# Kernel optimization log

Measured on AMD Instinct MI355X. Metric: run time of the kernel, lower is better.

The kernel has to match this reference:

```python
import jax, jax.numpy as jnp
import numpy as np

# ---- constants hard-coded in the torch module ----
NEG_EPS = 1e-30          # eps used in log clamps
TAU = 0.35               # near-field temperature (getattr default)
K0 = 128                 # near-field band width
C_EMBD, N_HEADS, RANK = 768, 12, 32
B, T = 1, 2048


def _lin(k, fin, fout):
    lim = 1.0 / np.sqrt(fin)
    return jax.random.uniform(k, (fin, fout), jnp.float32, -lim, lim)


def _bias(k, fin, fout):
    lim = 1.0 / np.sqrt(fin)
    return jax.random.uniform(k, (fout,), jnp.float32, -lim, lim)


def setup_inputs() -> dict:
    key = jax.random.key(0)
    ks = jax.random.split(key, 24)
    C, H, R = C_EMBD, N_HEADS, RANK
    return {
        "x": jax.random.normal(ks[0], (B, T, C), jnp.float32),
        "Wq_w": _lin(ks[1], C, C), "Wq_b": _bias(ks[2], C, C),
        "Wk_w": _lin(ks[3], C, C), "Wk_b": _bias(ks[4], C, C),
        "Wv_w": _lin(ks[5], C, C), "Wv_b": _bias(ks[6], C, C),
        "Wo_w": _lin(ks[7], C, C), "Wo_b": _bias(ks[8], C, C),
        "Pq_w": _lin(ks[9], C, R),
        "Pk_w": _lin(ks[10], C, R),
        "Pv_w": _lin(ks[11], C, R),
        "up_w": _lin(ks[12], R, C),
        "gate_u": jax.random.normal(ks[13], (H, C // H), jnp.float32),
        "gate_b": jnp.zeros((H,), jnp.float32),
        "Wz_w": _lin(ks[14], 4 * C, C), "Wz_b": _bias(ks[15], 4 * C, C),
    }


def reference(x, Wq_w, Wq_b, Wk_w, Wk_b, Wv_w, Wv_b, Wo_w, Wo_b,
              Pq_w, Pk_w, Pv_w, up_w, gate_u, gate_b, Wz_w, Wz_b):
    Bx, Tx, C = x.shape
    H = gate_u.shape[0]
    D = C // H
    R = Pq_w.shape[1]
    k0 = min(K0, Tx - 1)
    kernel = k0 + 1
    b_scalar = -np.log(max(Tx, 1)).astype(np.float32) if hasattr(np.log(1.0), 'astype') else -np.log(max(Tx, 1))
    b_scalar = jnp.float32(-np.log(max(Tx, 1)))

    # 0) projections + heads
    Q = x @ Wq_w + Wq_b
    K = x @ Wk_w + Wk_b
    V = x @ Wv_w + Wv_b
    heads = lambda z: z.reshape(Bx, Tx, H, D).transpose(0, 2, 1, 3)  # (B,H,T,D)
    Qh, Kh, Vh = heads(Q), heads(K), heads(V)

    idx = jnp.arange(Tx)
    causal = idx[None, :] <= idx[:, None]                  # (T,T)
    band = causal & ((idx[:, None] - idx[None, :]) <= k0)  # banded causal

    # 1) low-rank EA + sigmoid + LASER seed
    Qr, Kr, Vr = Q @ Pq_w, K @ Pk_w, V @ Pv_w              # (B,T,R)
    S = (Qr @ Kr.transpose(0, 2, 1)) * (1.0 / np.sqrt(R))  # (B,T,T)
    # masked logits were -1e9 -> sigmoid == 0 exactly in fp32
    A_seed = jnp.where(causal[None], jax.nn.sigmoid(S * S + b_scalar), 0.0)
    # running causal max over keys, per feature (== amax of causally masked keys)
    m_seed = jax.lax.cummax(Vr, axis=1)                    # (B,T,R)
    Yr = jnp.einsum('bij,bjr->bir', A_seed, jnp.exp(Vr)) * jnp.exp(-m_seed)
    H0 = (jnp.log(jnp.maximum(Yr, NEG_EPS)) + m_seed) @ up_w  # (B,T,C)

    # 2a) near-field banded causal attention (cos^2 / tau, sigmoid, LASER)
    l2n = lambda z: z / jnp.maximum(jnp.linalg.norm(z, axis=-1, keepdims=True), 1e-12)
    cos = jnp.einsum('bhid,bhjd->bhij', l2n(Qh), l2n(Kh))  # (B,H,T,T)
    A_near = jnp.where(band[None, None], jax.nn.sigmoid(cos * cos / TAU + b_scalar), 0.0)
    # sliding-window (width kernel, past-only) max of V per feature
    m_near = jax.lax.reduce_window(
        Vh, -jnp.inf, jax.lax.max,
        window_dimensions=(1, 1, kernel, 1), window_strides=(1, 1, 1, 1),
        padding=[(0, 0), (0, 0), (kernel - 1, 0), (0, 0)])   # (B,H,T,D)
    V_exp = jnp.exp(Vh - m_near)
    Y_near = jnp.einsum('bhij,bhjd->bhid', A_near, V_exp)
    H_near = jnp.log(jnp.maximum(Y_near, NEG_EPS)) + m_near

    # 2b) far-field hierarchical levels: source truncates mid-loop; the
    # accumulator H_far_total_h is initialized to zeros -> contributes zero.
    Ht_h = H_near                                          # (B,H,T,D)

    # 3) head-wise sigmoid gating
    g = jax.nn.sigmoid(jnp.einsum('bhtd,hd->bht', Ht_h, gate_u) + gate_b[None, :, None])
    Ht_h = Ht_h * g[..., None]
    Htilde = Ht_h.transpose(0, 2, 1, 3).reshape(Bx, Tx, C)

    # 4) GRU blend (Wz consumes 4*C features)
    z = jax.nn.sigmoid(jnp.concatenate([x, H0, Htilde, H0 * Htilde], axis=-1) @ Wz_w + Wz_b)
    H_out = (1.0 - z) * H0 + z * Htilde
    return H_out @ Wo_w + Wo_b
```

## Files before the change

### kernel.cpp

```cpp
#include <hip/hip_runtime.h>
#include <math.h>

static constexpr float B_SCALAR    = -7.6246189861593985f;
static constexpr float INV_TAU     = 2.8571428571428571f;
static constexpr float INV_SQRT_R  = 0.17677669529663687f;

typedef __attribute__((ext_vector_type(8))) short bf16x8;
typedef __attribute__((ext_vector_type(4))) float f32x4;

__device__ __forceinline__ unsigned short f2b(float f) {
    union { float f; unsigned int u; } v; v.f = f;
    unsigned int r = v.u + 0x7fffu + ((v.u >> 16) & 1u);
    return (unsigned short)(r >> 16);
}

typedef const __attribute__((address_space(1))) unsigned int* gp1_t;
typedef __attribute__((address_space(3))) unsigned int* lp3_t;
__device__ __forceinline__ void gload16(const unsigned short* g, unsigned short* l) {
    __builtin_amdgcn_global_load_lds((gp1_t)g, (lp3_t)l, 16, 0, 0);
}

__device__ __forceinline__ bf16x8 frag128(const unsigned short* base, int row, int elem) {
    int byte = (row * 128 + elem * 2) ^ ((row & 7) << 4);
    return *(const bf16x8*)((const char*)base + byte);
}
__device__ __forceinline__ bf16x8 frag384(const unsigned short* base, int row, int elem) {
    int byte = (row * 384 + elem * 2) ^ ((row & 7) << 4);
    return *(const bf16x8*)((const char*)base + byte);
}

template<int MODE, int KZ>
__global__ __launch_bounds__(256) void gemm_mfma(
    const unsigned short* __restrict__ A0, const unsigned short* __restrict__ A1,
    const unsigned short* __restrict__ A2, const unsigned short* __restrict__ A3,
    const unsigned short* __restrict__ Bt, const float* __restrict__ bias,
    float* __restrict__ outf, unsigned short* __restrict__ outb,
    float* __restrict__ pbuf, int K, int ldo)
{
    __shared__ unsigned short As[2][64*64];
    __shared__ unsigned short Bs[2][128*64];
    const int tid = threadIdx.x;
    const int lane = tid & 63, wid = tid >> 6;
    const int wr = wid >> 1, wc = wid & 1;
    const int fr = lane & 15, fq = lane >> 4;
    const int n0 = blockIdx.x * 128, m0 = blockIdx.y * 64;
    const int kz = blockIdx.z;
    const int kslice = K / KZ;
    const int kbase = kz * kslice;
    const int nt = kslice / 64;

    f32x4 acc[2][4];
#pragma unroll
    for (int mi = 0; mi < 2; ++mi)
#pragma unroll
        for (int ni = 0; ni < 4; ++ni) acc[mi][ni] = (f32x4){0.f, 0.f, 0.f, 0.f};

    auto stage = [&](int buf, int k0) {
        const unsigned short* Ap;
        int k0l, ldA;
        if (MODE == 1) {
            int p = k0 / 768;
            Ap = (p == 0) ? A0 : (p == 1) ? A1 : (p == 2) ? A2 : A3;
            k0l = k0 - p * 768; ldA = 768;
        } else { Ap = A0; k0l = k0; ldA = K; }
#pragma unroll
        for (int i = 0; i < 2; ++i) {
            int cb = i * 256 + wid * 64, c = cb + lane;
            int r = c >> 3;
            int col = ((c & 7) ^ (r & 7)) * 8;
            gload16(Ap + (size_t)(m0 + r) * ldA + k0l + col, &As[buf][cb * 8]);
        }
#pragma unroll
        for (int i = 0; i < 4; ++i) {
            int cb = i * 256 + wid * 64, c = cb + lane;
            int r = c >> 3;
            int col = ((c & 7) ^ (r & 7)) * 8;
            gload16(Bt + (size_t)(n0 + r) * K + k0 + col, &Bs[buf][cb * 8]);
        }
    };

    stage(0, kbase);
    asm volatile("s_waitcnt vmcnt(0)" ::: "memory");
    __builtin_amdgcn_s_barrier();
    __builtin_amdgcn_sched_barrier(0);

    int cur = 0;
    for (int t = 0; t < nt; ++t) {
        if (t + 1 < nt) stage(cur ^ 1, kbase + (t + 1) * 64);
#pragma unroll
        for (int kk = 0; kk < 64; kk += 32) {
            bf16x8 af[2], bfr[4];
#pragma unroll
            for (int mi = 0; mi < 2; ++mi)
                af[mi] = frag128(As[cur], wr*32 + mi*16 + fr, kk + fq*8);
#pragma unroll
            for (int ni = 0; ni < 4; ++ni)
                bfr[ni] = frag128(Bs[cur], wc*64 + ni*16 + fr, kk + fq*8);
#pragma unroll
            for (int mi = 0; mi < 2; ++mi)
#pragma unroll
                for (int ni = 0; ni < 4; ++ni)
                    acc[mi][ni] = __builtin_amdgcn_mfma_f32_16x16x32_bf16(
                        af[mi], bfr[ni], acc[mi][ni], 0, 0, 0);
        }
        asm volatile("s_waitcnt vmcnt(0)" ::: "memory");
        __builtin_amdgcn_s_barrier();
        __builtin_amdgcn_sched_barrier(0);
        cur ^= 1;
    }
#pragma unroll
    for (int mi = 0; mi < 2; ++mi)
#pragma unroll
        for (int ni = 0; ni < 4; ++ni)
#pragma unroll
            for (int v = 0; v < 4; ++v) {
                int m = m0 + wr*32 + mi*16 + fq*4 + v;
                int n = n0 + wc*64 + ni*16 + fr;
                float val = acc[mi][ni][v];
                if (KZ > 1) {
                    pbuf[((size_t)kz * 2048 + m) * 768 + n] = val;
                } else {
                    float vv = val + bias[n];
                    outf[(size_t)m * ldo + n] = vv;
                    if (MODE == 0) outb[(size_t)m * ldo + n] = f2b(vv);
                }
            }
}

__global__ __launch_bounds__(256) void wz_combine(
    const float* __restrict__ pbuf, const float* __restrict__ bz,
    const float* __restrict__ h0, const float* __restrict__ htl,
    unsigned short* __restrict__ outb)
{
    int i = blockIdx.x * 256 + threadIdx.x;
    if (i >= 2048*768/4) return;
    float4 s = *(const float4*)&pbuf[i*4];
    float4 p1 = *(const float4*)&pbuf[1536*1024 + i*4];
    float4 p2 = *(const float4*)&pbuf[2*1536*1024 + i*4];
    float4 p3 = *(const float4*)&pbuf[3*1536*1024 + i*4];
    s.x += p1.x + p2.x + p3.x; s.y += p1.y + p2.y + p3.y;
    s.z += p1.z + p2.z + p3.z; s.w += p1.w + p2.w + p3.w;
    float4 b = *(const float4*)&bz[(i % 192) * 4];
    float4 a = *(const float4*)&h0[i*4];
    float4 t = *(const float4*)&htl[i*4];
    float z0 = 1.f/(1.f+expf(-(s.x+b.x))), z1 = 1.f/(1.f+expf(-(s.y+b.y)));
    float z2 = 1.f/(1.f+expf(-(s.z+b.z))), z3 = 1.f/(1.f+expf(-(s.w+b.w)));
    outb[i*4+0] = f2b((1.f-z0)*a.x + z0*t.x);
    outb[i*4+1] = f2b((1.f-z1)*a.y + z1*t.y);
    outb[i*4+2] = f2b((1.f-z2)*a.z + z2*t.z);
    outb[i*4+3] = f2b((1.f-z3)*a.w + z3*t.w);
}

__global__ __launch_bounds__(256) void wo_combine(
    const float* __restrict__ pbuf, const float* __restrict__ bo,
    float* __restrict__ out)
{
    int i = blockIdx.x * 256 + threadIdx.x;
    if (i >= 2048*768/4) return;
    float4 s = *(const float4*)&pbuf[i*4];
    float4 p1 = *(const float4*)&pbuf[1536*1024 + i*4];
    float4 b = *(const float4*)&bo[(i % 192) * 4];
    float4 o;
    o.x = s.x + p1.x + b.x; o.y = s.y + p1.y + b.y;
    o.z = s.z + p1.z + b.z; o.w = s.w + p1.w + b.w;
    *(float4*)&out[i*4] = o;
}

__global__ __launch_bounds__(256) void prep_all(
    const float* __restrict__ x, unsigned short* __restrict__ xb,
    const float* __restrict__ wq, const float* __restrict__ wk,
    const float* __restrict__ wv, unsigned short* __restrict__ wqkvT,
    const float* __restrict__ wz, unsigned short* __restrict__ wzT,
    const float* __restrict__ wo, unsigned short* __restrict__ woT,
    const float* __restrict__ pq, const float* __restrict__ pk,
    const float* __restrict__ pv, unsigned short* __restrict__ pT,
    const float* __restrict__ bq, const float* __restrict__ bk,
    const float* __restrict__ bv, float* __restrict__ bqkv)
{
    __shared__ float tile[32][33];
    int b = blockIdx.x;
    if (b < 1536) {
        int i = b * 256 + threadIdx.x;
        float4 v = *(const float4*)&x[i * 4];
        xb[i*4+0] = f2b(v.x); xb[i*4+1] = f2b(v.y);
        xb[i*4+2] = f2b(v.z); xb[i*4+3] = f2b(v.w);
        return;
    }
    b -= 1536;
    const float* src; unsigned short* dst; int K, N, tb;
    if (b < 1728) {
        int sel = b / 576;
        src = (sel == 0) ? wq : (sel == 1) ? wk : wv;
        dst = wqkvT + (size_t)sel * 768 * 768;
        K = 768; N = 768; tb = b - sel * 576;
    } else if (b < 4032) {
        src = wz; dst = wzT; K = 3072; N = 768; tb = b - 1728;
    } else if (b < 4608) {
        src = wo; dst = woT; K = 768; N = 768; tb = b - 4032;
    } else if (b < 4680) {
        int sel = (b - 4608) / 24;
        src = (sel == 0) ? pq : (sel == 1) ? pk : pv;
        dst = pT + (size_t)sel * 32 * 768;
        K = 768; N = 32; tb = (b - 4608) % 24;
    } else {
        int n = (b - 4680) * 256 + threadIdx.x;
        if (n < 2304)
            bqkv[n] = (n < 768) ? bq[n] : (n < 1536) ? bk[n - 768] : bv[n - 1536];
        return;
    }
    int kt = K / 32;
    int kb = (tb % kt) * 32, nb = (tb / kt) * 32;
    int tx = threadIdx.x & 31, ty = threadIdx.x >> 5;
#pragma unroll
    for (int s = 0; s < 32; s += 8)
        tile[ty + s][tx] = src[(size_t)(kb + ty + s) * N + nb + tx];
    __syncthreads();
#pragma unroll
    for (int s = 0; s < 32; s += 8)
        dst[(size_t)(nb + ty + s) * K + kb + tx] = f2b(tile[tx][ty + s]);
}

__global__ __launch_bounds__(256) void lowrank_mfma(
    const unsigned short* __restrict__ qkvb, const unsigned short* __restrict__ pT,
    float* __restrict__ pbuf)
{
    __shared__ unsigned short As[2][128*64];
    __shared__ unsigned short Bs[2][32*64];
    const int tid = threadIdx.x, lane = tid & 63, wid = tid >> 6;
    const int fr = lane & 15, fq = lane >> 4;
    const int m0 = blockIdx.x * 128;
    const int sel = blockIdx.y, kz = blockIdx.z;
    const int kbase = kz * 192;

    f32x4 acc[2][2];
#pragma unroll
    for (int mi = 0; mi < 2; ++mi)
#pragma unroll
        for (int ni = 0; ni < 2; ++ni) acc[mi][ni] = (f32x4){0.f,0.f,0.f,0.f};

    auto stage = [&](int buf, int k0) {
#pragma unroll
        for (int i = 0; i < 4; ++i) {
            int cb = i * 256 + wid * 64, c = cb + lane;
            int r = c >> 3, col = ((c & 7) ^ (r & 7)) * 8;
            gload16(qkvb + (size_t)(m0 + r) * 2304 + sel*768 + k0 + col, &As[buf][cb * 8]);
        }
        {
            int cb = wid * 64, c = cb + lane;
            int r = c >> 3, col = ((c & 7) ^ (r & 7)) * 8;
            gload16(pT + (size_t)sel * 32*768 + (size_t)r * 768 + k0 + col, &Bs[buf][cb * 8]);
        }
    };

    stage(0, kbase);
    asm volatile("s_waitcnt vmcnt(0)" ::: "memory");
    __builtin_amdgcn_s_barrier();
    __builtin_amdgcn_sched_barrier(0);

    int cur = 0;
    for (int t = 0; t < 3; ++t) {
        if (t + 1 < 3) stage(cur ^ 1, kbase + (t + 1) * 64);
#pragma unroll
        for (int kk = 0; kk < 64; kk += 32) {
            bf16x8 a[2], b[2];
#pragma unroll
            for (int mi = 0; mi < 2; ++mi)
                a[mi] = frag128(As[cur], wid*32 + mi*16 + fr, kk + fq*8);
#pragma unroll
            for (int ni = 0; ni < 2; ++ni)
                b[ni] = frag128(Bs[cur], ni*16 + fr, kk + fq*8);
#pragma unroll
            for (int mi = 0; mi < 2; ++mi)
#pragma unroll
                for (int ni = 0; ni < 2; ++ni)
                    acc[mi][ni] = __builtin_amdgcn_mfma_f32_16x16x32_bf16(
                        a[mi], b[ni], acc[mi][ni], 0, 0, 0);
        }
        asm volatile("s_waitcnt vmcnt(0)" ::: "memory");
        __builtin_amdgcn_s_barrier();
        __builtin_amdgcn_sched_barrier(0);
        cur ^= 1;
    }
#pragma unroll
    for (int mi = 0; mi < 2; ++mi)
#pragma unroll
        for (int ni = 0; ni < 2; ++ni)
#pragma unroll
            for (int v = 0; v < 4; ++v) {
                int m = m0 + wid*32 + mi*16 + fq*4 + v;
                int n = ni*16 + fr;
                pbuf[((size_t)(kz*3 + sel) * 2048 + m) * 32 + n] = acc[mi][ni][v];
            }
}

__global__ __launch_bounds__(256) void lowrank_post(
    const float* __restrict__ pbuf,
    unsigned short* __restrict__ qrb, unsigned short* __restrict__ krb,
    unsigned short* __restrict__ evtb, float* __restrict__ ms)
{
    int b = blockIdx.x, tid = threadIdx.x;
    if (b < 512) {
        int idx = b * 256 + tid;
        int sel = idx >> 16, rem = idx & 65535;
        float s = pbuf[(size_t)(0*3 + sel)*65536 + rem]
                + pbuf[(size_t)(1*3 + sel)*65536 + rem]
                + pbuf[(size_t)(2*3 + sel)*65536 + rem]
                + pbuf[(size_t)(3*3 + sel)*65536 + rem];
        if (sel == 0) qrb[rem] = f2b(s * INV_SQRT_R);
        else          krb[rem] = f2b(s);
        return;
    }
    __shared__ float part[256];
    int r = b - 512;
    int t0 = tid * 8;
    float sv[8], v[8];
    float run = -INFINITY;
#pragma unroll
    for (int e = 0; e < 8; ++e) {
        int t = t0 + e;
        float s = pbuf[(size_t)(0*3 + 2)*65536 + t*32 + r]
                + pbuf[(size_t)(1*3 + 2)*65536 + t*32 + r]
                + pbuf[(size_t)(2*3 + 2)*65536 + t*32 + r]
                + pbuf[(size_t)(3*3 + 2)*65536 + t*32 + r];
        sv[e] = s;
        run = fmaxf(run, s);
        v[e] = run;
    }
    part[tid] = run;
    __syncthreads();
    for (int off = 1; off < 256; off <<= 1) {
        float other = (tid >= off) ? part[tid - off] : -INFINITY;
        __syncthreads();
        part[tid] = fmaxf(part[tid], other);
        __syncthreads();
    }
    float excl = (tid > 0) ? part[tid - 1] : -INFINITY;
#pragma unroll
    for (int e = 0; e < 8; ++e) {
        int t = t0 + e;
        ms[t*32 + r] = fmaxf(v[e], excl);
        evtb[(size_t)r * 2048 + t] = f2b(expf(sv[e]));
    }
}

__global__ __launch_bounds__(256) void seed_mfma(
    const unsigned short* __restrict__ qrb, const unsigned short* __restrict__ krb,
    const unsigned short* __restrict__ evtb, float* __restrict__ partial)
{
    int it = blockIdx.x, jc = blockIdx.y;
    if (jc > it) return;
    const int i0 = it * 128, j0 = jc * 128;
    __shared__ unsigned short Qs[128*32];
    __shared__ unsigned short Ks[128*32];
    __shared__ unsigned short Es[32*128];
    __shared__ unsigned short Ps[128*128];
    const int tid = threadIdx.x, lane = tid & 63, wid = tid >> 6;
    const int fr = lane & 15, fq = lane >> 4;

#pragma unroll
    for (int s = 0; s < 2; ++s) {
        int cb = s * 256 + wid * 64;
        int c = cb + lane;
        int r = c >> 2, col = (c & 3) * 8;
        gload16(qrb + (size_t)(i0 + r) * 32 + col, &Qs[cb * 8]);
        gload16(krb + (size_t)(j0 + r) * 32 + col, &Ks[cb * 8]);
    }
#pragma unroll
    for (int s = 0; s < 2; ++s) {
        int c = s * 256 + tid;
        int rr = c >> 4, cc = c & 15;
        bf16x8 v = *(const bf16x8*)&evtb[(size_t)rr * 2048 + j0 + cc * 8];
        int byte = (rr * 256 + cc * 16) ^ ((rr & 7) << 4);
        *(bf16x8*)((char*)Es + byte) = v;
    }
    __syncthreads();

    const int wr = wid >> 1, wc = wid & 1;
    bf16x8 af[4], bk[4];
#pragma unroll
    for (int mi = 0; mi < 4; ++mi)
        af[mi] = *(const bf16x8*)&Qs[(wr*64 + mi*16 + fr)*32 + fq*8];
#pragma unroll
    for (int ni = 0; ni < 4; ++ni)
        bk[ni] = *(const bf16x8*)&Ks[(wc*64 + ni*16 + fr)*32 + fq*8];
#pragma unroll
    for (int mi = 0; mi < 4; ++mi)
#pragma unroll
        for (int ni = 0; ni < 4; ++ni) {
            f32x4 s4 = __builtin_amdgcn_mfma_f32_16x16x32_bf16(
                af[mi], bk[ni], (f32x4){0.f,0.f,0.f,0.f}, 0, 0, 0);
#pragma unroll
            for (int v = 0; v < 4; ++v) {
                int row = wr*64 + mi*16 + fq*4 + v;
                int col = wc*64 + ni*16 + fr;
                float a = 0.f;
                if (j0 + col <= i0 + row) {
                    float s = s4[v];
                    a = 1.f / (1.f + expf(-(s*s + B_SCALAR)));
                }
                int byte = (row * 256 + col * 2) ^ ((row & 7) << 4);
                *(unsigned short*)((char*)Ps + byte) = f2b(a);
            }
        }
    __syncthreads();

    f32x4 yacc[2][2];
#pragma unroll
    for (int mi = 0; mi < 2; ++mi)
#pragma unroll
        for (int nf = 0; nf < 2; ++nf) yacc[mi][nf] = (f32x4){0.f,0.f,0.f,0.f};
#pragma unroll
    for (int ks = 0; ks < 4; ++ks) {
        bf16x8 pa[2], eb[2];
#pragma unroll
        for (int mi = 0; mi < 2; ++mi) {
            int row = wid*32 + mi*16 + fr;
            int byte = (row * 256 + ks * 64 + fq * 16) ^ ((row & 7) << 4);
            pa[mi] = *(const bf16x8*)((const char*)Ps + byte);
        }
#pragma unroll
        for (int nf = 0; nf < 2; ++nf) {
            int rrow = nf*16 + fr;
            int byte = (rrow * 256 + ks * 64 + fq * 16) ^ ((rrow & 7) << 4);
            eb[nf] = *(const bf16x8*)((const char*)Es + byte);
        }
#pragma unroll
        for (int mi = 0; mi < 2; ++mi)
#pragma unroll
            for (int nf = 0; nf < 2; ++nf)
                yacc[mi][nf] = __builtin_amdgcn_mfma_f32_16x16x32_bf16(
                    pa[mi], eb[nf], yacc[mi][nf], 0, 0, 0);
    }
    float* pout = partial + ((size_t)(it*16 + jc) * 128) * 32;
#pragma unroll
    for (int mi = 0; mi < 2; ++mi)
#pragma unroll
        for (int nf = 0; nf < 2; ++nf)
#pragma unroll
            for (int v = 0; v < 4; ++v) {
                int row = wid*32 + mi*16 + fq*4 + v;
                int col = nf*16 + fr;
                pout[row*32 + col] = yacc[mi][nf][v];
            }
}

__global__ __launch_bounds__(256) void seed_up(
    const float* __restrict__ partial, const float* __restrict__ ms,
    const float* __restrict__ up, float* __restrict__ h0,
    unsigned short* __restrict__ h0b)
{
    __shared__ float ls[32];
    int t = blockIdx.x, tid = threadIdx.x;
    if (tid < 32) {
        int r = tid;
        int it = t >> 7, row = t & 127;
        float y = 0.f;
        for (int jjc = 0; jjc <= it; ++jjc)
            y += partial[(((size_t)(it*16 + jjc) * 128) + row) * 32 + r];
        float m = ms[t*32 + r];
        ls[r] = logf(fmaxf(y * expf(-m), 1e-30f)) + m;
    }
    __syncthreads();
    for (int c = tid; c < 768; c += 256) {
        float acc = 0.f;
#pragma unroll
        for (int rr = 0; rr < 32; ++rr) acc = fmaf(ls[rr], up[rr*768 + c], acc);
        h0[(size_t)t*768 + c] = acc;
        h0b[(size_t)t*768 + c] = f2b(acc);
    }
}

__global__ __launch_bounds__(256) void norms_slide(
    const float* __restrict__ qkv,
    unsigned short* __restrict__ qhatb, unsigned short* __restrict__ khatb,
    float* __restrict__ mnear, unsigned short* __restrict__ vexptb)
{
    __shared__ float vs[192][64];
    int b = blockIdx.x, tid = threadIdx.x;
    if (b < 6144) {
        int w = b * 4 + (tid >> 6);
        int lane = tid & 63;
        int t = w / 12, h = w - t * 12;
        float q = qkv[t*2304 + h*64 + lane];
        float k = qkv[t*2304 + 768 + h*64 + lane];
        float sq = q*q, sk = k*k;
#pragma unroll
        for (int off = 32; off; off >>= 1) { sq += __shfl_xor(sq, off); sk += __shfl_xor(sk, off); }
        float iq = 1.f / fmaxf(sqrtf(sq), 1e-12f);
        float ik = 1.f / fmaxf(sqrtf(sk), 1e-12f);
        qhatb[(size_t)t*768 + h*64 + lane] = f2b(q * iq);
        khatb[(size_t)t*768 + h*64 + lane] = f2b(k * ik);
        return;
    }
    b -= 6144;
    int c0 = (b % 12) * 64, t0 = (b / 12) * 64;
#pragma unroll
    for (int s = 0; s < 12; ++s) {
        int idx = tid + s * 256;
        int rr = idx >> 4, c4 = (idx & 15) * 4;
        int t = t0 - 128 + rr;
        float4 v4;
        if (t < 0) v4 = make_float4(-INFINITY, -INFINITY, -INFINITY, -INFINITY);
        else       v4 = *(const float4*)&qkv[t*2304 + 1536 + c0 + c4];
        *(float4*)&vs[rr][c4] = v4;
    }
    __syncthreads();
    int c = tid & 63, tg = tid >> 6;
    const int TG = tg * 16;
    float core = -INFINITY;
    for (int s = TG + 15; s <= TG + 128; ++s) core = fmaxf(core, vs[s][c]);
    float head[16], tail[16];
    head[15] = -INFINITY;
    float hs = -INFINITY;
#pragma unroll
    for (int u = 14; u >= 0; --u) { hs = fmaxf(hs, vs[TG + u][c]); head[u] = hs; }
    tail[0] = -INFINITY;
    float ts = -INFINITY;
#pragma unroll
    for (int u = 1; u <= 15; ++u) { ts = fmaxf(ts, vs[TG + 128 + u][c]); tail[u] = ts; }
#pragma unroll
    for (int u = 0; u < 16; ++u) {
        int tl = TG + u;
        float m = fmaxf(fmaxf(core, head[u]), tail[u]);
        float v = vs[tl + 128][c];
        int t = t0 + tl;
        mnear[(size_t)t*768 + c0 + c] = m;
        vexptb[(size_t)(c0 + c) * 2048 + t] = f2b(expf(v - m));
    }
}

__global__ __launch_bounds__(256) void near_fused(
    const unsigned short* __restrict__ qhatb, const unsigned short* __restrict__ khatb,
    const unsigned short* __restrict__ vexptb, const float* __restrict__ mnear,
    const float* __restrict__ gu, const float* __restrict__ gb,
    const float* __restrict__ h0, float* __restrict__ hn,
    unsigned short* __restrict__ htlb, unsigned short* __restrict__ prodb)
{
    __shared__ unsigned short Qs[64*64];
    __shared__ unsigned short KPs[192*64];
    __shared__ unsigned short Vst[64*192];
    const int it = blockIdx.x, hh = blockIdx.y;
    const int i0 = it * 64;
    const int tid = threadIdx.x, lane = tid & 63, wid = tid >> 6;
    const int fr = lane & 15, fq = lane >> 4;

#pragma unroll
    for (int i = 0; i < 2; ++i) {
        int cb = i * 256 + wid * 64, c = cb + lane;
        int r = c >> 3, col = ((c & 7) ^ (r & 7)) * 8;
        gload16(qhatb + (size_t)(i0 + r) * 768 + hh*64 + col, &Qs[cb * 8]);
    }
#pragma unroll
    for (int i = 0; i < 6; ++i) {
        int cb = i * 256 + wid * 64, c = cb + lane;
        int r = c >> 3, col = ((c & 7) ^ (r & 7)) * 8;
        int j = i0 - 128 + r; if (j < 0) j = 0;
        gload16(khatb + (size_t)j * 768 + hh*64 + col, &KPs[cb * 8]);
    }
#pragma unroll
    for (int i = 0; i < 6; ++i) {
        int cb = i * 256 + wid * 64, c = cb + lane;
        int d = c / 24, cc = c - d * 24;
        int ccp = (cc & 24) | ((cc & 7) ^ (d & 7));
        int t = i0 - 128 + ccp * 8; if (t < 0) t = 0;
        gload16(vexptb + (size_t)(hh*64 + d) * 2048 + t, &Vst[cb * 8]);
    }
    __syncthreads();

    f32x4 sacc[4][3];
#pragma unroll
    for (int mi = 0; mi < 4; ++mi)
#pragma unroll
        for (int ni = 0; ni < 3; ++ni) sacc[mi][ni] = (f32x4){0.f,0.f,0.f,0.f};
#pragma unroll
    for (int kt = 0; kt < 2; ++kt) {
        int kk = kt * 32;
        bf16x8 qa[4], kb[3];
#pragma unroll
        for (int mi = 0; mi < 4; ++mi)
            qa[mi] = frag128(Qs, mi*16 + fr, kk + fq*8);
#pragma unroll
        for (int ni = 0; ni < 3; ++ni)
            kb[ni] = frag128(KPs, wid*48 + ni*16 + fr, kk + fq*8);
#pragma unroll
        for (int mi = 0; mi < 4; ++mi)
#pragma unroll
            for (int ni = 0; ni < 3; ++ni)
                sacc[mi][ni] = __builtin_amdgcn_mfma_f32_16x16x32_bf16(
                    qa[mi], kb[ni], sacc[mi][ni], 0, 0, 0);
    }
    __syncthreads();

#pragma unroll
    for (int mi = 0; mi < 4; ++mi)
#pragma unroll
        for (int ni = 0; ni < 3; ++ni)
#pragma unroll
            for (int v = 0; v < 4; ++v) {
                int il = mi*16 + fq*4 + v;
                int jl = wid*48 + ni*16 + fr;
                float s = sacc[mi][ni][v];
                float a = 0.f;
                if (jl >= il && jl <= il + 128 && (i0 - 128 + jl) >= 0)
                    a = 1.f / (1.f + expf(-(s*s*INV_TAU + B_SCALAR)));
                int byte = (il * 384 + jl * 2) ^ ((il & 7) << 4);
                *(unsigned short*)((char*)KPs + byte) = f2b(a);
            }
    __syncthreads();

    f32x4 yacc[4];
#pragma unroll
    for (int nf = 0; nf < 4; ++nf) yacc[nf] = (f32x4){0.f,0.f,0.f,0.f};
#pragma unroll
    for (int ks = 0; ks < 6; ++ks) {
        int kk = ks * 32;
        bf16x8 pa = frag384(KPs, wid*16 + fr, kk + fq*8);
        bf16x8 vb[4];
#pragma unroll
        for (int nf = 0; nf < 4; ++nf)
            vb[nf] = frag384(Vst, nf*16 + fr, kk + fq*8);
#pragma unroll
        for (int nf = 0; nf < 4; ++nf)
            yacc[nf] = __builtin_amdgcn_mfma_f32_16x16x32_bf16(pa, vb[nf], yacc[nf], 0, 0, 0);
    }

    float hv[4][4];
    float sp[4] = {0.f, 0.f, 0.f, 0.f};
#pragma unroll
    for (int nf = 0; nf < 4; ++nf) {
        int d = nf*16 + fr;
        float guv = gu[hh*64 + d];
#pragma unroll
        for (int v = 0; v < 4; ++v) {
            int row = wid*16 + fq*4 + v;
            float y = yacc[nf][v];
            float h = logf(fmaxf(y, 1e-30f)) + mnear[(size_t)(i0 + row)*768 + hh*64 + d];
            hv[nf][v] = h;
            sp[v] = fmaf(h, guv, sp[v]);
        }
    }
#pragma unroll
    for (int off = 1; off < 16; off <<= 1) {
#pragma unroll
        for (int v = 0; v < 4; ++v) sp[v] += __shfl_xor(sp[v], off);
    }
    float gbh = gb[hh];
#pragma unroll
    for (int v = 0; v < 4; ++v) sp[v] = 1.f / (1.f + expf(-(sp[v] + gbh)));
#pragma unroll
    for (int nf = 0; nf < 4; ++nf)
#pragma unroll
        for (int v = 0; v < 4; ++v) {
            int row = wid*16 + fq*4 + v;
            int d = nf*16 + fr;
            size_t idx = (size_t)(i0 + row)*768 + hh*64 + d;
            float htl = hv[nf][v] * sp[v];
            hn[idx] = htl;
            htlb[idx] = f2b(htl);
            prodb[idx] = f2b(h0[idx] * htl);
        }
}

extern "C" void kernel_launch(void* const* d_in, const int* in_sizes, int n_in,
                              void* d_out, int out_size, void* d_ws, size_t ws_size,
                              hipStream_t stream)
{
    const float* x  = (const float*)d_in[0];
    const float* wq = (const float*)d_in[1];  const float* bq = (const float*)d_in[2];
    const float* wk = (const float*)d_in[3];  const float* bk = (const float*)d_in[4];
    const float* wv = (const float*)d_in[5];  const float* bv = (const float*)d_in[6];
    const float* wo = (const float*)d_in[7];  const float* bo = (const float*)d_in[8];
    const float* pq = (const float*)d_in[9];  const float* pk = (const float*)d_in[10];
    const float* pv = (const float*)d_in[11];
    const float* up = (const float*)d_in[12];
    const float* gu = (const float*)d_in[13]; const float* gb = (const float*)d_in[14];
    const float* wz = (const float*)d_in[15]; const float* bz = (const float*)d_in[16];
    float* out = (float*)d_out;

    float* w = (float*)d_ws;
    float* qkv  = w; w += 2048*2304;
    float* ms   = w; w += 2048*32;
    float* h0   = w; w += 2048*768;
    float* mnear= w; w += 2048*768;
    float* hn   = w; w += 2048*768;
    float* partial = w; w += 16*16*128*32;
    float* pgemm = w; w += 4*2048*768;
    float* plr   = w; w += 4*3*2048*32;
    float* bqkv = w; w += 2304;
    unsigned short* xb     = (unsigned short*)w; w += 2048*768/2;
    unsigned short* qkvb   = (unsigned short*)w; w += 2048*2304/2;
    unsigned short* wqkvT  = (unsigned short*)w; w += 2304*768/2;
    unsigned short* wzT    = (unsigned short*)w; w += 768*3072/2;
    unsigned short* woT    = (unsigned short*)w; w += 768*768/2;
    unsigned short* pT     = (unsigned short*)w; w += 3*32*768/2;
    unsigned short* h0b    = (unsigned short*)w; w += 2048*768/2;
    unsigned short* htlb   = (unsigned short*)w; w += 2048*768/2;
    unsigned short* prodb  = (unsigned short*)w; w += 2048*768/2;
    unsigned short* houtb  = (unsigned short*)w; w += 2048*768/2;
    unsigned short* qrb    = (unsigned short*)w; w += 2048*32/2;
    unsigned short* krb    = (unsigned short*)w; w += 2048*32/2;
    unsigned short* evtb   = (unsigned short*)w; w += 32*2048/2;
    unsigned short* qhatb  = (unsigned short*)w; w += 2048*768/2;
    unsigned short* khatb  = (unsigned short*)w; w += 2048*768/2;
    unsigned short* vexptb = (unsigned short*)w; w += 768*2048/2;

    prep_all<<<6225, 256, 0, stream>>>(x, xb, wq, wk, wv, wqkvT, wz, wzT,
                                       wo, woT, pq, pk, pv, pT, bq, bk, bv, bqkv);

    gemm_mfma<0,1><<<dim3(18,32,1), 256, 0, stream>>>(xb, nullptr, nullptr, nullptr,
        wqkvT, bqkv, qkv, qkvb, nullptr, 768, 2304);

    lowrank_mfma<<<dim3(16,3,4), 256, 0, stream>>>(qkvb, pT, plr);
    lowrank_post<<<544, 256, 0, stream>>>(plr, qrb, krb, evtb, ms);
    seed_mfma<<<dim3(16,16), 256, 0, stream>>>(qrb, krb, evtb, partial);
    seed_up<<<2048, 256, 0, stream>>>(partial, ms, up, h0, h0b);

    norms_slide<<<6528, 256, 0, stream>>>(qkv, qhatb, khatb, mnear, vexptb);
    near_fused<<<dim3(32,12), 256, 0, stream>>>(qhatb, khatb, vexptb, mnear,
                                                gu, gb, h0, hn, htlb, prodb);

    gemm_mfma<1,4><<<dim3(6,32,4), 256, 0, stream>>>(xb, h0b, htlb, prodb,
        wzT, nullptr, nullptr, nullptr, pgemm, 3072, 768);
    wz_combine<<<1536, 256, 0, stream>>>(pgemm, bz, h0, hn, houtb);
    gemm_mfma<2,2><<<dim3(6,32,2), 256, 0, stream>>>(houtb, nullptr, nullptr, nullptr,
        woT, nullptr, nullptr, nullptr, pgemm, 768, 768);
    wo_combine<<<1536, 256, 0, stream>>>(pgemm, bo, out);
}
```

Baseline: 149.3 us.

## Pack independent kernels, compute H0*Htilde on the fly, drop Wo split-K

Merges the low-rank projection with the norm/sliding-max kernel, and the seed kernel with the near-field kernel, into single packed launches so independent work runs concurrently. Removes the prodb buffer by computing H0*Htilde in the Wz GEMM A-tile stage with regular loads and LDS stores. Switches the Wo GEMM to a single k-slice with a fused bias epilogue, dropping wo_combine, and adds an XCD-aware block swizzle to the GEMMs. This trades fewer launches and less memory traffic for a slower non-async staging path in part of the Wz GEMM and less parallelism in the Wo GEMM.

```diff
diff --git a/kernel.cpp b/kernel.cpp
--- a/kernel.cpp
+++ b/kernel.cpp
@@ -13,6 +13,9 @@
     unsigned int r = v.u + 0x7fffu + ((v.u >> 16) & 1u);
     return (unsigned short)(r >> 16);
 }
+__device__ __forceinline__ float b2f(unsigned short u) {
+    union { unsigned int i; float f; } v; v.i = ((unsigned int)u) << 16; return v.f;
+}
 
 typedef const __attribute__((address_space(1))) unsigned int* gp1_t;
 typedef __attribute__((address_space(3))) unsigned int* lp3_t;
@@ -32,7 +35,7 @@
 template<int MODE, int KZ>
 __global__ __launch_bounds__(256) void gemm_mfma(
     const unsigned short* __restrict__ A0, const unsigned short* __restrict__ A1,
-    const unsigned short* __restrict__ A2, const unsigned short* __restrict__ A3,
+    const unsigned short* __restrict__ A2,
     const unsigned short* __restrict__ Bt, const float* __restrict__ bias,
     float* __restrict__ outf, unsigned short* __restrict__ outb,
     float* __restrict__ pbuf, int K, int ldo)
@@ -43,7 +46,10 @@
     const int lane = tid & 63, wid = tid >> 6;
     const int wr = wid >> 1, wc = wid & 1;
     const int fr = lane & 15, fq = lane >> 4;
-    const int n0 = blockIdx.x * 128, m0 = blockIdx.y * 64;
+    const int lin = blockIdx.y * gridDim.x + blockIdx.x;
+    const int chunk = (gridDim.x * gridDim.y) >> 3;
+    const int sw = (lin & 7) * chunk + (lin >> 3);
+    const int n0 = (sw / gridDim.y) * 128, m0 = (sw % gridDim.y) * 64;
     const int kz = blockIdx.z;
     const int kslice = K / KZ;
     const int kbase = kz * kslice;
@@ -56,19 +62,35 @@
         for (int ni = 0; ni < 4; ++ni) acc[mi][ni] = (f32x4){0.f, 0.f, 0.f, 0.f};
 
     auto stage = [&](int buf, int k0) {
-        const unsigned short* Ap;
-        int k0l, ldA;
-        if (MODE == 1) {
-            int p = k0 / 768;
-            Ap = (p == 0) ? A0 : (p == 1) ? A1 : (p == 2) ? A2 : A3;
-            k0l = k0 - p * 768; ldA = 768;
-        } else { Ap = A0; k0l = k0; ldA = K; }
-#pragma unroll
-        for (int i = 0; i < 2; ++i) {
-            int cb = i * 256 + wid * 64, c = cb + lane;
-            int r = c >> 3;
-            int col = ((c & 7) ^ (r & 7)) * 8;
-            gload16(Ap + (size_t)(m0 + r) * ldA + k0l + col, &As[buf][cb * 8]);
+        if (MODE == 1 && k0 >= 2304) {
+            int k0l = k0 - 2304;
+#pragma unroll
+            for (int i = 0; i < 2; ++i) {
+                int cb = i * 256 + wid * 64, c = cb + lane;
+                int r = c >> 3, col = ((c & 7) ^ (r & 7)) * 8;
+                bf16x8 a8 = *(const bf16x8*)&A1[(size_t)(m0 + r) * 768 + k0l + col];
+                bf16x8 b8 = *(const bf16x8*)&A2[(size_t)(m0 + r) * 768 + k0l + col];
+                bf16x8 p8;
+#pragma unroll
+                for (int e = 0; e < 8; ++e)
+                    p8[e] = (short)f2b(b2f((unsigned short)a8[e]) * b2f((unsigned short)b8[e]));
+                *(bf16x8*)&As[buf][(size_t)c * 8] = p8;
+            }
+        } else {
+            const unsigned short* Ap;
+            int k0l, ldA;
+            if (MODE == 1) {
+                int p = k0 / 768;
+                Ap = (p == 0) ? A0 : (p == 1) ? A1 : A2;
+                k0l = k0 - p * 768; ldA = 768;
+            } else { Ap = A0; k0l = k0; ldA = K; }
+#pragma unroll
+            for (int i = 0; i < 2; ++i) {
+                int cb = i * 256 + wid * 64, c = cb + lane;
+                int r = c >> 3;
+                int col = ((c & 7) ^ (r & 7)) * 8;
+                gload16(Ap + (size_t)(m0 + r) * ldA + k0l + col, &As[buf][cb * 8]);
+            }
         }
 #pragma unroll
         for (int i = 0; i < 4; ++i) {
@@ -80,7 +102,7 @@
     };
 
     stage(0, kbase);
-    asm volatile("s_waitcnt vmcnt(0)" ::: "memory");
+    asm volatile("s_waitcnt vmcnt(0) lgkmcnt(0)" ::: "memory");
     __builtin_amdgcn_s_barrier();
     __builtin_amdgcn_sched_barrier(0);
 
@@ -103,7 +125,7 @@
                     acc[mi][ni] = __builtin_amdgcn_mfma_f32_16x16x32_bf16(
                         af[mi], bfr[ni], acc[mi][ni], 0, 0, 0);
         }
-        asm volatile("s_waitcnt vmcnt(0)" ::: "memory");
+        asm volatile("s_waitcnt vmcnt(0) lgkmcnt(0)" ::: "memory");
         __builtin_amdgcn_s_barrier();
         __builtin_amdgcn_sched_barrier(0);
         cur ^= 1;
@@ -149,21 +171,6 @@
     outb[i*4+1] = f2b((1.f-z1)*a.y + z1*t.y);
     outb[i*4+2] = f2b((1.f-z2)*a.z + z2*t.z);
     outb[i*4+3] = f2b((1.f-z3)*a.w + z3*t.w);
-}
-
-__global__ __launch_bounds__(256) void wo_combine(
-    const float* __restrict__ pbuf, const float* __restrict__ bo,
-    float* __restrict__ out)
-{
-    int i = blockIdx.x * 256 + threadIdx.x;
-    if (i >= 2048*768/4) return;
-    float4 s = *(const float4*)&pbuf[i*4];
-    float4 p1 = *(const float4*)&pbuf[1536*1024 + i*4];
-    float4 b = *(const float4*)&bo[(i % 192) * 4];
-    float4 o;
-    o.x = s.x + p1.x + b.x; o.y = s.y + p1.y + b.y;
-    o.z = s.z + p1.z + b.z; o.w = s.w + p1.w + b.w;
-    *(float4*)&out[i*4] = o;
 }
 
 __global__ __launch_bounds__(256) void prep_all(
@@ -220,16 +227,16 @@
         dst[(size_t)(nb + ty + s) * K + kb + tx] = f2b(tile[tx][ty + s]);
 }
 
-__global__ __launch_bounds__(256) void lowrank_mfma(
+__device__ void lowrank_body(int b, unsigned char* smem,
     const unsigned short* __restrict__ qkvb, const unsigned short* __restrict__ pT,
     float* __restrict__ pbuf)
 {
-    __shared__ unsigned short As[2][128*64];
-    __shared__ unsigned short Bs[2][32*64];
+    unsigned short (*As)[128*64] = (unsigned short(*)[128*64])smem;
+    unsigned short (*Bs)[32*64]  = (unsigned short(*)[32*64])(smem + 32768);
     const int tid = threadIdx.x, lane = tid & 63, wid = tid >> 6;
     const int fr = lane & 15, fq = lane >> 4;
-    const int m0 = blockIdx.x * 128;
-    const int sel = blockIdx.y, kz = blockIdx.z;
+    const int m0 = (b & 15) * 128;
+    const int sel = (b >> 4) % 3, kz = b / 48;
     const int kbase = kz * 192;
 
     f32x4 acc[2][2];
@@ -262,19 +269,19 @@
         if (t + 1 < 3) stage(cur ^ 1, kbase + (t + 1) * 64);
 #pragma unroll
         for (int kk = 0; kk < 64; kk += 32) {
-            bf16x8 a[2], b[2];
+            bf16x8 a[2], bb[2];
 #pragma unroll
             for (int mi = 0; mi < 2; ++mi)
                 a[mi] = frag128(As[cur], wid*32 + mi*16 + fr, kk + fq*8);
 #pragma unroll
             for (int ni = 0; ni < 2; ++ni)
-                b[ni] = frag128(Bs[cur], ni*16 + fr, kk + fq*8);
+                bb[ni] = frag128(Bs[cur], ni*16 + fr, kk + fq*8);
 #pragma unroll
             for (int mi = 0; mi < 2; ++mi)
 #pragma unroll
                 for (int ni = 0; ni < 2; ++ni)
                     acc[mi][ni] = __builtin_amdgcn_mfma_f32_16x16x32_bf16(
-                        a[mi], b[ni], acc[mi][ni], 0, 0, 0);
+                        a[mi], bb[ni], acc[mi][ni], 0, 0, 0);
         }
         asm volatile("s_waitcnt vmcnt(0)" ::: "memory");
         __builtin_amdgcn_s_barrier();
@@ -291,6 +298,77 @@
                 int n = ni*16 + fr;
                 pbuf[((size_t)(kz*3 + sel) * 2048 + m) * 32 + n] = acc[mi][ni][v];
             }
+}
+
+__device__ void norms_slide_body(int b, unsigned char* smem,
+    const float* __restrict__ qkv,
+    unsigned short* __restrict__ qhatb, unsigned short* __restrict__ khatb,
+    float* __restrict__ mnear, unsigned short* __restrict__ vexptb)
+{
+    int tid = threadIdx.x;
+    if (b < 6144) {
+        int w = b * 4 + (tid >> 6);
+        int lane = tid & 63;
+        int t = w / 12, h = w - t * 12;
+        float q = qkv[t*2304 + h*64 + lane];
+        float k = qkv[t*2304 + 768 + h*64 + lane];
+        float sq = q*q, sk = k*k;
+#pragma unroll
+        for (int off = 32; off; off >>= 1) { sq += __shfl_xor(sq, off); sk += __shfl_xor(sk, off); }
+        float iq = 1.f / fmaxf(sqrtf(sq), 1e-12f);
+        float ik = 1.f / fmaxf(sqrtf(sk), 1e-12f);
+        qhatb[(size_t)t*768 + h*64 + lane] = f2b(q * iq);
+        khatb[(size_t)t*768 + h*64 + lane] = f2b(k * ik);
+        return;
+    }
+    b -= 6144;
+    float (*vs)[64] = (float(*)[64])smem;
+    int c0 = (b % 12) * 64, t0 = (b / 12) * 64;
+#pragma unroll
+    for (int s = 0; s < 12; ++s) {
+        int idx = tid + s * 256;
+        int rr = idx >> 4, c4 = (idx & 15) * 4;
+        int t = t0 - 128 + rr;
+        float4 v4;
+        if (t < 0) v4 = make_float4(-INFINITY, -INFINITY, -INFINITY, -INFINITY);
+        else       v4 = *(const float4*)&qkv[t*2304 + 1536 + c0 + c4];
+        *(float4*)&vs[rr][c4] = v4;
+    }
+    __syncthreads();
+    int c = tid & 63, tg = tid >> 6;
+    const int TG = tg * 16;
+    float core = -INFINITY;
+    for (int s = TG + 15; s <= TG + 128; ++s) core = fmaxf(core, vs[s][c]);
+    float head[16], tail[16];
+    head[15] = -INFINITY;
+    float hs = -INFINITY;
+#pragma unroll
+    for (int u = 14; u >= 0; --u) { hs = fmaxf(hs, vs[TG + u][c]); head[u] = hs; }
+    tail[0] = -INFINITY;
+    float ts = -INFINITY;
+#pragma unroll
+    for (int u = 1; u <= 15; ++u) { ts = fmaxf(ts, vs[TG + 128 + u][c]); tail[u] = ts; }
+#pragma unroll
+    for (int u = 0; u < 16; ++u) {
+        int tl = TG + u;
+        float m = fmaxf(fmaxf(core, head[u]), tail[u]);
+        float v = vs[tl + 128][c];
+        int t = t0 + tl;
+        mnear[(size_t)t*768 + c0 + c] = m;
+        vexptb[(size_t)(c0 + c) * 2048 + t] = f2b(expf(v - m));
+    }
+}
+
+__global__ __launch_bounds__(256) void lrns_pack(
+    const unsigned short* __restrict__ qkvb, const unsigned short* __restrict__ pT,
+    float* __restrict__ plr, const float* __restrict__ qkv,
+    unsigned short* __restrict__ qhatb, unsigned short* __restrict__ khatb,
+    float* __restrict__ mnear, unsigned short* __restrict__ vexptb)
+{
+    __shared__ unsigned char smem[49152];
+    int b = blockIdx.x;
+    if (b < 192) lowrank_body(b, smem, qkvb, pT, plr);
+    else         norms_slide_body(b - 192, smem, qkv, qhatb, khatb, mnear, vexptb);
 }
 
 __global__ __launch_bounds__(256) void lowrank_post(
@@ -343,17 +421,15 @@
     }
 }
 
-__global__ __launch_bounds__(256) void seed_mfma(
+__device__ void seed_body(int it, int jc, unsigned char* smem,
     const unsigned short* __restrict__ qrb, const unsigned short* __restrict__ krb,
     const unsigned short* __restrict__ evtb, float* __restrict__ partial)
 {
-    int it = blockIdx.x, jc = blockIdx.y;
-    if (jc > it) return;
     const int i0 = it * 128, j0 = jc * 128;
-    __shared__ unsigned short Qs[128*32];
-    __shared__ unsigned short Ks[128*32];
-    __shared__ unsigned short Es[32*128];
-    __shared__ unsigned short Ps[128*128];
+    unsigned short* Qs = (unsigned short*)smem;
+    unsigned short* Ks = (unsigned short*)(smem + 8192);
+    unsigned short* Es = (unsigned short*)(smem + 16384);
+    unsigned short* Ps = (unsigned short*)(smem + 24576);
     const int tid = threadIdx.x, lane = tid & 63, wid = tid >> 6;
     const int fr = lane & 15, fq = lane >> 4;
 
@@ -444,6 +520,156 @@
             }
 }
 
+__device__ void near_body(int it, int hh, unsigned char* smem,
+    const unsigned short* __restrict__ qhatb, const unsigned short* __restrict__ khatb,
+    const unsigned short* __restrict__ vexptb, const float* __restrict__ mnear,
+    const float* __restrict__ gu, const float* __restrict__ gb,
+    float* __restrict__ hn, unsigned short* __restrict__ htlb)
+{
+    unsigned short* Qs  = (unsigned short*)smem;
+    unsigned short* KPs = (unsigned short*)(smem + 8192);
+    unsigned short* Vst = (unsigned short*)(smem + 32768);
+    const int i0 = it * 64;
+    const int tid = threadIdx.x, lane = tid & 63, wid = tid >> 6;
+    const int fr = lane & 15, fq = lane >> 4;
+
+#pragma unroll
+    for (int i = 0; i < 2; ++i) {
+        int cb = i * 256 + wid * 64, c = cb + lane;
+        int r = c >> 3, col = ((c & 7) ^ (r & 7)) * 8;
+        gload16(qhatb + (size_t)(i0 + r) * 768 + hh*64 + col, &Qs[cb * 8]);
+    }
+#pragma unroll
+    for (int i = 0; i < 6; ++i) {
+        int cb = i * 256 + wid * 64, c = cb + lane;
+        int r = c >> 3, col = ((c & 7) ^ (r & 7)) * 8;
+        int j = i0 - 128 + r; if (j < 0) j = 0;
+        gload16(khatb + (size_t)j * 768 + hh*64 + col, &KPs[cb * 8]);
+    }
+#pragma unroll
+    for (int i = 0; i < 6; ++i) {
+        int cb = i * 256 + wid * 64, c = cb + lane;
+        int d = c / 24, cc = c - d * 24;
+        int ccp = (cc & 24) | ((cc & 7) ^ (d & 7));
+        int t = i0 - 128 + ccp * 8; if (t < 0) t = 0;
+        gload16(vexptb + (size_t)(hh*64 + d) * 2048 + t, &Vst[cb * 8]);
+    }
+    __syncthreads();
+
+    f32x4 sacc[4][3];
+#pragma unroll
+    for (int mi = 0; mi < 4; ++mi)
+#pragma unroll
+        for (int ni = 0; ni < 3; ++ni) sacc[mi][ni] = (f32x4){0.f,0.f,0.f,0.f};
+#pragma unroll
+    for (int kt = 0; kt < 2; ++kt) {
+        int kk = kt * 32;
+        bf16x8 qa[4], kb[3];
+#pragma unroll
+        for (int mi = 0; mi < 4; ++mi)
+            qa[mi] = frag128(Qs, mi*16 + fr, kk + fq*8);
+#pragma unroll
+        for (int ni = 0; ni < 3; ++ni)
+            kb[ni] = frag128(KPs, wid*48 + ni*16 + fr, kk + fq*8);
+#pragma unroll
+        for (int mi = 0; mi < 4; ++mi)
+#pragma unroll
+            for (int ni = 0; ni < 3; ++ni)
+                sacc[mi][ni] = __builtin_amdgcn_mfma_f32_16x16x32_bf16(
+                    qa[mi], kb[ni], sacc[mi][ni], 0, 0, 0);
+    }
+    __syncthreads();
+
+#pragma unroll
+    for (int mi = 0; mi < 4; ++mi)
+#pragma unroll
+        for (int ni = 0; ni < 3; ++ni)
+#pragma unroll
+            for (int v = 0; v < 4; ++v) {
+                int il = mi*16 + fq*4 + v;
+                int jl = wid*48 + ni*16 + fr;
+                float s = sacc[mi][ni][v];
+                float a = 0.f;
+                if (jl >= il && jl <= il + 128 && (i0 - 128 + jl) >= 0)
+                    a = 1.f / (1.f + expf(-(s*s*INV_TAU + B_SCALAR)));
+                int byte = (il * 384 + jl * 2) ^ ((il & 7) << 4);
+                *(unsigned short*)((char*)KPs + byte) = f2b(a);
+            }
+    __syncthreads();
+
+    f32x4 yacc[4];
+#pragma unroll
+    for (int nf = 0; nf < 4; ++nf) yacc[nf] = (f32x4){0.f,0.f,0.f,0.f};
+#pragma unroll
+    for (int ks = 0; ks < 6; ++ks) {
+        int kk = ks * 32;
+        bf16x8 pa = frag384(KPs, wid*16 + fr, kk + fq*8);
+        bf16x8 vb[4];
+#pragma unroll
+        for (int nf = 0; nf < 4; ++nf)
+            vb[nf] = frag384(Vst, nf*16 + fr, kk + fq*8);
+#pragma unroll
+        for (int nf = 0; nf < 4; ++nf)
+            yacc[nf] = __builtin_amdgcn_mfma_f32_16x16x32_bf16(pa, vb[nf], yacc[nf], 0, 0, 0);
+    }
+
+    float hv[4][4];
+    float sp[4] = {0.f, 0.f, 0.f, 0.f};
+#pragma unroll
+    for (int nf = 0; nf < 4; ++nf) {
+        int d = nf*16 + fr;
+        float guv = gu[hh*64 + d];
+#pragma unroll
+        for (int v = 0; v < 4; ++v) {
+            int row = wid*16 + fq*4 + v;
+            float y = yacc[nf][v];
+            float h = logf(fmaxf(y, 1e-30f)) + mnear[(size_t)(i0 + row)*768 + hh*64 + d];
+            hv[nf][v] = h;
+            sp[v] = fmaf(h, guv, sp[v]);
+        }
+    }
+#pragma unroll
+    for (int off = 1; off < 16; off <<= 1) {
+#pragma unroll
+        for (int v = 0; v < 4; ++v) sp[v] += __shfl_xor(sp[v], off);
+    }
+    float gbh = gb[hh];
+#pragma unroll
+    for (int v = 0; v < 4; ++v) sp[v] = 1.f / (1.f + expf(-(sp[v] + gbh)));
+#pragma unroll
+    for (int nf = 0; nf < 4; ++nf)
+#pragma unroll
+        for (int v = 0; v < 4; ++v) {
+            int row = wid*16 + fq*4 + v;
+            int d = nf*16 + fr;
+            size_t idx = (size_t)(i0 + row)*768 + hh*64 + d;
+            float htl = hv[nf][v] * sp[v];
+            hn[idx] = htl;
+            htlb[idx] = f2b(htl);
+        }
+}
+
+__global__ __launch_bounds__(256) void seednear_pack(
+    const unsigned short* __restrict__ qrb, const unsigned short* __restrict__ krb,
+    const unsigned short* __restrict__ evtb, float* __restrict__ partial,
+    const unsigned short* __restrict__ qhatb, const unsigned short* __restrict__ khatb,
+    const unsigned short* __restrict__ vexptb, const float* __restrict__ mnear,
+    const float* __restrict__ gu, const float* __restrict__ gb,
+    float* __restrict__ hn, unsigned short* __restrict__ htlb)
+{
+    __shared__ unsigned char smem[57344];
+    int b = blockIdx.x;
+    if (b < 256) {
+        int it = b >> 4, jc = b & 15;
+        if (jc > it) return;
+        seed_body(it, jc, smem, qrb, krb, evtb, partial);
+    } else {
+        int idx = b - 256;
+        near_body(idx & 31, idx >> 5, smem, qhatb, khatb, vexptb, mnear,
+                  gu, gb, hn, htlb);
+    }
+}
+
 __global__ __launch_bounds__(256) void seed_up(
     const float* __restrict__ partial, const float* __restrict__ ms,
     const float* __restrict__ up, float* __restrict__ h0,
@@ -468,197 +694,6 @@
         h0[(size_t)t*768 + c] = acc;
         h0b[(size_t)t*768 + c] = f2b(acc);
     }
-}
-
-__global__ __launch_bounds__(256) void norms_slide(
-    const float* __restrict__ qkv,
-    unsigned short* __restrict__ qhatb, unsigned short* __restrict__ khatb,
-    float* __restrict__ mnear, unsigned short* __restrict__ vexptb)
-{
-    __shared__ float vs[192][64];
-    int b = blockIdx.x, tid = threadIdx.x;
-    if (b < 6144) {
-        int w = b * 4 + (tid >> 6);
-        int lane = tid & 63;
-        int t = w / 12, h = w - t * 12;
-        float q = qkv[t*2304 + h*64 + lane];
-        float k = qkv[t*2304 + 768 + h*64 + lane];
-        float sq = q*q, sk = k*k;
-#pragma unroll
-        for (int off = 32; off; off >>= 1) { sq += __shfl_xor(sq, off); sk += __shfl_xor(sk, off); }
-        float iq = 1.f / fmaxf(sqrtf(sq), 1e-12f);
-        float ik = 1.f / fmaxf(sqrtf(sk), 1e-12f);
-        qhatb[(size_t)t*768 + h*64 + lane] = f2b(q * iq);
-        khatb[(size_t)t*768 + h*64 + lane] = f2b(k * ik);
-        return;
-    }
-    b -= 6144;
-    int c0 = (b % 12) * 64, t0 = (b / 12) * 64;
-#pragma unroll
-    for (int s = 0; s < 12; ++s) {
-        int idx = tid + s * 256;
-        int rr = idx >> 4, c4 = (idx & 15) * 4;
-        int t = t0 - 128 + rr;
-        float4 v4;
-        if (t < 0) v4 = make_float4(-INFINITY, -INFINITY, -INFINITY, -INFINITY);
-        else       v4 = *(const float4*)&qkv[t*2304 + 1536 + c0 + c4];
-        *(float4*)&vs[rr][c4] = v4;
-    }
-    __syncthreads();
-    int c = tid & 63, tg = tid >> 6;
-    const int TG = tg * 16;
-    float core = -INFINITY;
-    for (int s = TG + 15; s <= TG + 128; ++s) core = fmaxf(core, vs[s][c]);
-    float head[16], tail[16];
-    head[15] = -INFINITY;
-    float hs = -INFINITY;
-#pragma unroll
-    for (int u = 14; u >= 0; --u) { hs = fmaxf(hs, vs[TG + u][c]); head[u] = hs; }
-    tail[0] = -INFINITY;
-    float ts = -INFINITY;
-#pragma unroll
-    for (int u = 1; u <= 15; ++u) { ts = fmaxf(ts, vs[TG + 128 + u][c]); tail[u] = ts; }
-#pragma unroll
-    for (int u = 0; u < 16; ++u) {
-        int tl = TG + u;
-        float m = fmaxf(fmaxf(core, head[u]), tail[u]);
-        float v = vs[tl + 128][c];
-        int t = t0 + tl;
-        mnear[(size_t)t*768 + c0 + c] = m;
-        vexptb[(size_t)(c0 + c) * 2048 + t] = f2b(expf(v - m));
-    }
-}
-
-__global__ __launch_bounds__(256) void near_fused(
-    const unsigned short* __restrict__ qhatb, const unsigned short* __restrict__ khatb,
-    const unsigned short* __restrict__ vexptb, const float* __restrict__ mnear,
-    const float* __restrict__ gu, const float* __restrict__ gb,
-    const float* __restrict__ h0, float* __restrict__ hn,
-    unsigned short* __restrict__ htlb, unsigned short* __restrict__ prodb)
-{
-    __shared__ unsigned short Qs[64*64];
-    __shared__ unsigned short KPs[192*64];
-    __shared__ unsigned short Vst[64*192];
-    const int it = blockIdx.x, hh = blockIdx.y;
-    const int i0 = it * 64;
-    const int tid = threadIdx.x, lane = tid & 63, wid = tid >> 6;
-    const int fr = lane & 15, fq = lane >> 4;
-
-#pragma unroll
-    for (int i = 0; i < 2; ++i) {
-        int cb = i * 256 + wid * 64, c = cb + lane;
-        int r = c >> 3, col = ((c & 7) ^ (r & 7)) * 8;
-        gload16(qhatb + (size_t)(i0 + r) * 768 + hh*64 + col, &Qs[cb * 8]);
-    }
-#pragma unroll
-    for (int i = 0; i < 6; ++i) {
-        int cb = i * 256 + wid * 64, c = cb + lane;
-        int r = c >> 3, col = ((c & 7) ^ (r & 7)) * 8;
-        int j = i0 - 128 + r; if (j < 0) j = 0;
-        gload16(khatb + (size_t)j * 768 + hh*64 + col, &KPs[cb * 8]);
-    }
-#pragma unroll
-    for (int i = 0; i < 6; ++i) {
-        int cb = i * 256 + wid * 64, c = cb + lane;
-        int d = c / 24, cc = c - d * 24;
-        int ccp = (cc & 24) | ((cc & 7) ^ (d & 7));
-        int t = i0 - 128 + ccp * 8; if (t < 0) t = 0;
-        gload16(vexptb + (size_t)(hh*64 + d) * 2048 + t, &Vst[cb * 8]);
-    }
-    __syncthreads();
-
-    f32x4 sacc[4][3];
-#pragma unroll
-    for (int mi = 0; mi < 4; ++mi)
-#pragma unroll
-        for (int ni = 0; ni < 3; ++ni) sacc[mi][ni] = (f32x4){0.f,0.f,0.f,0.f};
-#pragma unroll
-    for (int kt = 0; kt < 2; ++kt) {
-        int kk = kt * 32;
-        bf16x8 qa[4], kb[3];
-#pragma unroll
-        for (int mi = 0; mi < 4; ++mi)
-            qa[mi] = frag128(Qs, mi*16 + fr, kk + fq*8);
-#pragma unroll
-        for (int ni = 0; ni < 3; ++ni)
-            kb[ni] = frag128(KPs, wid*48 + ni*16 + fr, kk + fq*8);
-#pragma unroll
-        for (int mi = 0; mi < 4; ++mi)
-#pragma unroll
-            for (int ni = 0; ni < 3; ++ni)
-                sacc[mi][ni] = __builtin_amdgcn_mfma_f32_16x16x32_bf16(
-                    qa[mi], kb[ni], sacc[mi][ni], 0, 0, 0);
-    }
-    __syncthreads();
-
-#pragma unroll
-    for (int mi = 0; mi < 4; ++mi)
-#pragma unroll
-        for (int ni = 0; ni < 3; ++ni)
-#pragma unroll
-            for (int v = 0; v < 4; ++v) {
-                int il = mi*16 + fq*4 + v;
-                int jl = wid*48 + ni*16 + fr;
-                float s = sacc[mi][ni][v];
-                float a = 0.f;
-                if (jl >= il && jl <= il + 128 && (i0 - 128 + jl) >= 0)
-                    a = 1.f / (1.f + expf(-(s*s*INV_TAU + B_SCALAR)));
-                int byte = (il * 384 + jl * 2) ^ ((il & 7) << 4);
-                *(unsigned short*)((char*)KPs + byte) = f2b(a);
-            }
-    __syncthreads();
-
-    f32x4 yacc[4];
-#pragma unroll
-    for (int nf = 0; nf < 4; ++nf) yacc[nf] = (f32x4){0.f,0.f,0.f,0.f};
-#pragma unroll
-    for (int ks = 0; ks < 6; ++ks) {
-        int kk = ks * 32;
-        bf16x8 pa = frag384(KPs, wid*16 + fr, kk + fq*8);
-        bf16x8 vb[4];
-#pragma unroll
-        for (int nf = 0; nf < 4; ++nf)
-            vb[nf] = frag384(Vst, nf*16 + fr, kk + fq*8);
-#pragma unroll
-        for (int nf = 0; nf < 4; ++nf)
-            yacc[nf] = __builtin_amdgcn_mfma_f32_16x16x32_bf16(pa, vb[nf], yacc[nf], 0, 0, 0);
-    }
-
-    float hv[4][4];
-    float sp[4] = {0.f, 0.f, 0.f, 0.f};
-#pragma unroll
-    for (int nf = 0; nf < 4; ++nf) {
-        int d = nf*16 + fr;
-        float guv = gu[hh*64 + d];
-#pragma unroll
-        for (int v = 0; v < 4; ++v) {
-            int row = wid*16 + fq*4 + v;
-            float y = yacc[nf][v];
-            float h = logf(fmaxf(y, 1e-30f)) + mnear[(size_t)(i0 + row)*768 + hh*64 + d];
-            hv[nf][v] = h;
-            sp[v] = fmaf(h, guv, sp[v]);
-        }
-    }
-#pragma unroll
-    for (int off = 1; off < 16; off <<= 1) {
-#pragma unroll
-        for (int v = 0; v < 4; ++v) sp[v] += __shfl_xor(sp[v], off);
-    }
-    float gbh = gb[hh];
-#pragma unroll
-    for (int v = 0; v < 4; ++v) sp[v] = 1.f / (1.f + expf(-(sp[v] + gbh)));
-#pragma unroll
-    for (int nf = 0; nf < 4; ++nf)
-#pragma unroll
-        for (int v = 0; v < 4; ++v) {
-            int row = wid*16 + fq*4 + v;
-            int d = nf*16 + fr;
-            size_t idx = (size_t)(i0 + row)*768 + hh*64 + d;
-            float htl = hv[nf][v] * sp[v];
-            hn[idx] = htl;
-            htlb[idx] = f2b(htl);
-            prodb[idx] = f2b(h0[idx] * htl);
-        }
 }
 
 extern "C" void kernel_launch(void* const* d_in, const int* in_sizes, int n_in,
@@ -695,7 +730,6 @@
     unsigned short* pT     = (unsigned short*)w; w += 3*32*768/2;
     unsigned short* h0b    = (unsigned short*)w; w += 2048*768/2;
     unsigned short* htlb   = (unsigned short*)w; w += 2048*768/2;
-    unsigned short* prodb  = (unsigned short*)w; w += 2048*768/2;
     unsigned short* houtb  = (unsigned short*)w; w += 2048*768/2;
     unsigned short* qrb    = (unsigned short*)w; w += 2048*32/2;
     unsigned short* krb    = (unsigned short*)w; w += 2048*32/2;
@@ -707,22 +741,23 @@
     prep_all<<<6225, 256, 0, stream>>>(x, xb, wq, wk, wv, wqkvT, wz, wzT,
                                        wo, woT, pq, pk, pv, pT, bq, bk, bv, bqkv);
 
-    gemm_mfma<0,1><<<dim3(18,32,1), 256, 0, stream>>>(xb, nullptr, nullptr, nullptr,
+    gemm_mfma<0,1><<<dim3(18,32,1), 256, 0, stream>>>(xb, nullptr, nullptr,
         wqkvT, bqkv, qkv, qkvb, nullptr, 768, 2304);
 
-    lowrank_mfma<<<dim3(16,3,4), 256, 0, stream>>>(qkvb, pT, plr);
+    lrns_pack<<<6720, 256, 0, stream>>>(qkvb, pT, plr, qkv, qhatb, khatb, mnear, vexptb);
+
     lowrank_post<<<544, 256, 0, stream>>>(plr, qrb, krb, evtb, ms);
-    seed_mfma<<<dim3(16,16), 256, 0, stream>>>(qrb, krb, evtb, partial);
+
+    seednear_pack<<<640, 256, 0, stream>>>(qrb, krb, evtb, partial,
+        qhatb, khatb, vexptb, mnear, gu, gb, hn, htlb);
+
     seed_up<<<2048, 256, 0, stream>>>(partial, ms, up, h0, h0b);
 
-    norms_slide<<<6528, 256, 0, stream>>>(qkv, qhatb, khatb, mnear, vexptb);
-    near_fused<<<dim3(32,12), 256, 0, stream>>>(qhatb, khatb, vexptb, mnear,
-                                                gu, gb, h0, hn, htlb, prodb);
-
-    gemm_mfma<1,4><<<dim3(6,32,4), 256, 0, stream>>>(xb, h0b, htlb, prodb,
+    gemm_mfma<1,4><<<dim3(6,32,4), 256, 0, stream>>>(xb, h0b, htlb,
         wzT, nullptr, nullptr, nullptr, pgemm, 3072, 768);
+
     wz_combine<<<1536, 256, 0, stream>>>(pgemm, bz, h0, hn, houtb);
-    gemm_mfma<2,2><<<dim3(6,32,2), 256, 0, stream>>>(houtb, nullptr, nullptr, nullptr,
-        woT, nullptr, nullptr, nullptr, pgemm, 768, 768);
-    wo_combine<<<1536, 256, 0, stream>>>(pgemm, bo, out);
-}
+
+    gemm_mfma<2,1><<<dim3(6,32,1), 256, 0, stream>>>(houtb, nullptr, nullptr,
+        woT, bo, out, nullptr, nullptr, 768, 768);
+}
```

After: 148.9 us. About the same (-0.3%).
